# Performance work log

Measured on AMD Instinct MI355X. Metric: run time of the kernel, lower is better.

Reference implementation:

```python
import jax, jax.numpy as jnp
import numpy as np

# Module hyperparameters (match init_kwargs)
D, H1, H2, H3 = 64, 16, 16, 16
N = 65536  # batch size


def _masks():
    # Block-diagonal masks in (in, out) orientation; matches torch m1..m4
    eye = np.eye(D, dtype=np.float32)
    m1 = np.kron(eye, np.ones((1, H1), np.float32))    # (D, H1*D)
    m2 = np.kron(eye, np.ones((H1, H2), np.float32))   # (H1*D, H2*D)
    m3 = np.kron(eye, np.ones((H2, H3), np.float32))   # (H2*D, H3*D)
    m4 = np.kron(eye, np.ones((H3, 1), np.float32))    # (H3*D, D)
    return tuple(jnp.asarray(m) for m in (m1, m2, m3, m4))


def setup_inputs() -> dict:
    key = jax.random.key(0)
    ks = jax.random.split(key, 8)
    def init_w(k, fan_in, fan_out):
        # kaiming-uniform-like scale (nn.Linear default ~ U(-1/sqrt(fan_in), 1/sqrt(fan_in)))
        bound = 1.0 / np.sqrt(fan_in)
        return jax.random.uniform(k, (fan_in, fan_out), jnp.float32, -bound, bound)
    x = jax.random.normal(ks[0], (N, D), jnp.float32)
    W1 = init_w(ks[1], D, H1 * D)
    W2 = init_w(ks[2], H1 * D, H2 * D)
    W3 = init_w(ks[3], H2 * D, H3 * D)
    W4 = init_w(ks[4], H3 * D, D)
    Wp = init_w(ks[5], D, 1)
    bp = jax.random.uniform(ks[6], (1,), jnp.float32, -1.0 / np.sqrt(D), 1.0 / np.sqrt(D))
    return {"x": x, "W1": W1, "W2": W2, "W3": W3, "W4": W4, "Wp": Wp, "bp": bp}


def reference(x, W1, W2, W3, W4, Wp, bp):
    M1, M2, M3, M4 = _masks()
    # SparseLayer: masked dense linear (bias=False), then ELU
    o1 = jax.nn.elu(x @ (W1 * M1))    # (N, H1*D)
    o2 = jax.nn.elu(o1 @ (W2 * M2))   # (N, H2*D)
    o3 = jax.nn.elu(o2 @ (W3 * M3))   # (N, H3*D)
    out = o3 @ (W4 * M4)              # (N, D) per-feature GAM contributions
    pred1 = out @ Wp + bp             # (N, 1) final prediction (Identity act)
    return pred1, out
```

## Files before the change

kernel.cpp:

```cpp
#include <hip/hip_runtime.h>


#define BLK 256
#define FG 8
#define SPT 2
#define DTOT 64

__device__ __forceinline__ float getc(float4 v, int i) {
    switch (i & 3) {
        case 0: return v.x;
        case 1: return v.y;
        case 2: return v.z;
        default: return v.w;
    }
}
#define GET16(h0, h1, h2, h3, i) \
    getc((i) < 4 ? (h0) : (i) < 8 ? (h1) : (i) < 12 ? (h2) : (h3), (i))

__device__ __forceinline__ float4 mul4(float s, float4 w) {
    float4 r;
    r.x = s * w.x; r.y = s * w.y; r.z = s * w.z; r.w = s * w.w;
    return r;
}
__device__ __forceinline__ float4 fma4(float s, float4 w, float4 a) {
    a.x = fmaf(s, w.x, a.x); a.y = fmaf(s, w.y, a.y);
    a.z = fmaf(s, w.z, a.z); a.w = fmaf(s, w.w, a.w);
    return a;
}
__device__ __forceinline__ float elu_f(float v) {
    return v > 0.0f ? v : (__expf(v) - 1.0f);
}
__device__ __forceinline__ float4 elu4(float4 v) {
    float4 r;
    r.x = elu_f(v.x); r.y = elu_f(v.y); r.z = elu_f(v.z); r.w = elu_f(v.w);
    return r;
}
__device__ __forceinline__ float dot4(float4 a, float4 b) {
    return fmaf(a.x, b.x, fmaf(a.y, b.y, fmaf(a.z, b.z, a.w * b.w)));
}
__device__ __forceinline__ float4 zero4() {
    float4 r; r.x = 0.f; r.y = 0.f; r.z = 0.f; r.w = 0.f; return r;
}

__device__ __forceinline__ void stage_weights(
    int tid, int d0,
    const float* __restrict__ W1, const float* __restrict__ W2,
    const float* __restrict__ W3, const float* __restrict__ W4,
    float (*w1s)[16], float (*w2s)[16][16], float (*w3s)[16][16], float (*w4s)[16])
{
    if (tid < 128) {
        int dd = tid >> 4, j = tid & 15;
        int d = d0 + dd;
        w1s[dd][j] = W1[d * 1024 + d * 16 + j];
    } else {
        int t = tid - 128;
        int dd = t >> 4, i = t & 15;
        int d = d0 + dd;
        w4s[dd][i] = W4[(d * 16 + i) * 64 + d];
    }
    for (int idx = tid; idx < FG * 256; idx += BLK) {
        int dd = idx >> 8, r = idx & 255;
        int i = r >> 4, j = r & 15;
        int d = d0 + dd;
        size_t base = (size_t)(d * 16 + i) * 1024 + d * 16 + j;
        w2s[dd][i][j] = W2[base];
        w3s[dd][i][j] = W3[base];
    }
}

#define LAYER16(ws)                                                        \
    {                                                                      \
        float4 a0 = zero4(), a1 = zero4(), a2 = zero4(), a3 = zero4();     \
        float4 b0 = zero4(), b1 = zero4(), b2 = zero4(), b3 = zero4();     \
        _Pragma("unroll")                                                  \
        for (int i = 0; i < 16; ++i) {                                     \
            const float hai = GET16(ha0, ha1, ha2, ha3, i);                \
            const float hbi = GET16(hb0, hb1, hb2, hb3, i);                \
            const float4* wp = (const float4*)((ws) + i * 16);             \
            const float4 q0 = wp[0], q1 = wp[1], q2 = wp[2], q3 = wp[3];   \
            a0 = fma4(hai, q0, a0); a1 = fma4(hai, q1, a1);                \
            a2 = fma4(hai, q2, a2); a3 = fma4(hai, q3, a3);                \
            b0 = fma4(hbi, q0, b0); b1 = fma4(hbi, q1, b1);                \
            b2 = fma4(hbi, q2, b2); b3 = fma4(hbi, q3, b3);                \
        }                                                                  \
        ha0 = elu4(a0); ha1 = elu4(a1); ha2 = elu4(a2); ha3 = elu4(a3);    \
        hb0 = elu4(b0); hb1 = elu4(b1); hb2 = elu4(b2); hb3 = elu4(b3);    \
    }


__global__ __launch_bounds__(256) void transpose_in(
    const float* __restrict__ x, float* __restrict__ xt, int nsamp)
{
    __shared__ float t[64][65];
    const int s0 = blockIdx.x * 64;
    const int c = threadIdx.x & 63;
    const int r0 = threadIdx.x >> 6;
    for (int i = r0; i < 64; i += 4)
        t[i][c] = x[(size_t)(s0 + i) * DTOT + c];
    __syncthreads();
    for (int d = r0; d < 64; d += 4)
        xt[(size_t)d * nsamp + s0 + c] = t[c][d];
}

__global__ __launch_bounds__(BLK, 4) void gam_main_t(
    const float* __restrict__ xt, const float* __restrict__ W1,
    const float* __restrict__ W2, const float* __restrict__ W3,
    const float* __restrict__ W4, float* __restrict__ ot, int nsamp)
{
    __shared__ float w1s[FG][16];
    __shared__ float w2s[FG][16][16];
    __shared__ float w3s[FG][16][16];
    __shared__ float w4s[FG][16];

    const int tid = threadIdx.x;
    const int g = blockIdx.x & 7;
    const int chunk = blockIdx.x >> 3;
    const int d0 = g * FG;

    stage_weights(tid, d0, W1, W2, W3, W4, w1s, w2s, w3s, w4s);
    __syncthreads();

    const int s0 = chunk * (BLK * SPT) + tid;
    const int s1 = s0 + BLK;
    if (s0 >= nsamp) return;

    for (int dd = 0; dd < FG; ++dd) {
        const int d = d0 + dd;
        const size_t rowb = (size_t)d * nsamp;
        const float xv0 = xt[rowb + s0];
        const float xv1 = xt[rowb + s1];

        const float4* w1p = (const float4*)&w1s[dd][0];
        const float4 u0 = w1p[0], u1 = w1p[1], u2 = w1p[2], u3 = w1p[3];
        float4 ha0 = elu4(mul4(xv0, u0)), ha1 = elu4(mul4(xv0, u1));
        float4 ha2 = elu4(mul4(xv0, u2)), ha3 = elu4(mul4(xv0, u3));
        float4 hb0 = elu4(mul4(xv1, u0)), hb1 = elu4(mul4(xv1, u1));
        float4 hb2 = elu4(mul4(xv1, u2)), hb3 = elu4(mul4(xv1, u3));

        LAYER16(&w2s[dd][0][0]);
        LAYER16(&w3s[dd][0][0]);

        const float4* w4p = (const float4*)&w4s[dd][0];
        const float4 q0 = w4p[0], q1 = w4p[1], q2 = w4p[2], q3 = w4p[3];
        const float oa = (dot4(ha0, q0) + dot4(ha1, q1)) +
                         (dot4(ha2, q2) + dot4(ha3, q3));
        const float ob = (dot4(hb0, q0) + dot4(hb1, q1)) +
                         (dot4(hb2, q2) + dot4(hb3, q3));
        ot[rowb + s0] = oa;
        ot[rowb + s1] = ob;
    }
}

__global__ __launch_bounds__(256) void finish(
    const float* __restrict__ ot, const float* __restrict__ Wp,
    const float* __restrict__ bp, float* __restrict__ out,
    float* __restrict__ pred, int nsamp)
{
    __shared__ float t[64][65];
    __shared__ float wps[64];
    const int s0 = blockIdx.x * 64;
    const int c = threadIdx.x & 63;
    const int r0 = threadIdx.x >> 6;
    if (threadIdx.x < 64) wps[threadIdx.x] = Wp[threadIdx.x];
    for (int d = r0; d < 64; d += 4)
        t[d][c] = ot[(size_t)d * nsamp + s0 + c];
    __syncthreads();
    for (int i = r0; i < 64; i += 4)
        out[(size_t)(s0 + i) * DTOT + c] = t[c][i];
    if (r0 == 0) {
        float p = bp[0];
#pragma unroll
        for (int d = 0; d < 64; ++d)
            p = fmaf(t[d][c], wps[d], p);
        pred[s0 + c] = p;
    }
}


__global__ __launch_bounds__(BLK, 4) void gam_main_direct(
    const float* __restrict__ x, const float* __restrict__ W1,
    const float* __restrict__ W2, const float* __restrict__ W3,
    const float* __restrict__ W4, float* __restrict__ out, int nsamp)
{
    __shared__ float w1s[FG][16];
    __shared__ float w2s[FG][16][16];
    __shared__ float w3s[FG][16][16];
    __shared__ float w4s[FG][16];

    const int tid = threadIdx.x;
    const int g = blockIdx.x & 7;
    const int chunk = blockIdx.x >> 3;
    const int d0 = g * FG;

    stage_weights(tid, d0, W1, W2, W3, W4, w1s, w2s, w3s, w4s);
    __syncthreads();

    const int s0 = chunk * (BLK * SPT) + tid;
    const int s1 = s0 + BLK;
    if (s0 >= nsamp) return;

    for (int dd = 0; dd < FG; ++dd) {
        const int d = d0 + dd;
        const float xv0 = x[(size_t)s0 * DTOT + d];
        const float xv1 = x[(size_t)s1 * DTOT + d];

        const float4* w1p = (const float4*)&w1s[dd][0];
        const float4 u0 = w1p[0], u1 = w1p[1], u2 = w1p[2], u3 = w1p[3];
        float4 ha0 = elu4(mul4(xv0, u0)), ha1 = elu4(mul4(xv0, u1));
        float4 ha2 = elu4(mul4(xv0, u2)), ha3 = elu4(mul4(xv0, u3));
        float4 hb0 = elu4(mul4(xv1, u0)), hb1 = elu4(mul4(xv1, u1));
        float4 hb2 = elu4(mul4(xv1, u2)), hb3 = elu4(mul4(xv1, u3));

        LAYER16(&w2s[dd][0][0]);
        LAYER16(&w3s[dd][0][0]);

        const float4* w4p = (const float4*)&w4s[dd][0];
        const float4 q0 = w4p[0], q1 = w4p[1], q2 = w4p[2], q3 = w4p[3];
        out[(size_t)s0 * DTOT + d] = (dot4(ha0, q0) + dot4(ha1, q1)) +
                                     (dot4(ha2, q2) + dot4(ha3, q3));
        out[(size_t)s1 * DTOT + d] = (dot4(hb0, q0) + dot4(hb1, q1)) +
                                     (dot4(hb2, q2) + dot4(hb3, q3));
    }
}

__global__ __launch_bounds__(BLK) void gam_pred_direct(
    const float* __restrict__ out, const float* __restrict__ Wp,
    const float* __restrict__ bp, float* __restrict__ pred, int nsamp)
{
    int gid = blockIdx.x * BLK + threadIdx.x;
    int wave = gid >> 6, lane = gid & 63;
    int sub = lane >> 4, li = lane & 15;
    int s = wave * 4 + sub;
    if (s >= nsamp) return;
    float4 wv = ((const float4*)Wp)[li];
    float4 v = ((const float4*)(out + (size_t)s * DTOT))[li];
    float p = v.x * wv.x + v.y * wv.y + v.z * wv.z + v.w * wv.w;
    p += __shfl_xor(p, 1);
    p += __shfl_xor(p, 2);
    p += __shfl_xor(p, 4);
    p += __shfl_xor(p, 8);
    if (li == 0) pred[s] = p + bp[0];
}

extern "C" void kernel_launch(void* const* d_in, const int* in_sizes, int n_in,
                              void* d_out, int out_size, void* d_ws, size_t ws_size,
                              hipStream_t stream) {
    const float* x  = (const float*)d_in[0];
    const float* W1 = (const float*)d_in[1];
    const float* W2 = (const float*)d_in[2];
    const float* W3 = (const float*)d_in[3];
    const float* W4 = (const float*)d_in[4];
    const float* Wp = (const float*)d_in[5];
    const float* bp = (const float*)d_in[6];

    const int nsamp = in_sizes[0] / DTOT;
    float* pred = (float*)d_out;
    float* outm = pred + nsamp;

    const size_t need = (size_t)2 * nsamp * DTOT * sizeof(float);
    if (ws_size >= need) {
        float* xt = (float*)d_ws;
        float* ot = xt + (size_t)nsamp * DTOT;
        transpose_in<<<dim3(nsamp / 64), dim3(256), 0, stream>>>(x, xt, nsamp);
        gam_main_t<<<dim3((nsamp / (BLK * SPT)) * 8), dim3(BLK), 0, stream>>>(
            xt, W1, W2, W3, W4, ot, nsamp);
        finish<<<dim3(nsamp / 64), dim3(256), 0, stream>>>(
            ot, Wp, bp, outm, pred, nsamp);
    } else {
        int chunks = nsamp / (BLK * SPT);
        gam_main_direct<<<dim3(chunks * 8), dim3(BLK), 0, stream>>>(
            x, W1, W2, W3, W4, outm, nsamp);
        int nthreads = (nsamp / 4) * 64;
        gam_pred_direct<<<dim3((nthreads + BLK - 1) / BLK), dim3(BLK), 0, stream>>>(
            outm, Wp, bp, pred, nsamp);
    }
}
```

Measured before the change: 94.92 us.

## Read block-diagonal weights directly from global memory instead of LDS staging

The transposed-path main kernel no longer stages the per-feature weight blocks into shared memory behind a barrier. Instead each thread loads W1/W2/W3/W4 through uniform global loads (scalar/cached) inside the loop. It also halves features per block (4 instead of 8), which doubles the grid, drops the occupancy hint from launch bounds and disables unrolling of the feature loop. This removes the staging cost and the syncthreads, but adds repeated global/cache reads of weights on the hot inner loop, including strided W4 loads.

```diff
diff --git a/kernel.cpp b/kernel.cpp
--- a/kernel.cpp
+++ b/kernel.cpp
@@ -2,8 +2,8 @@
 
 
 #define BLK 256
+#define FGF 4
 #define FG 8
-#define SPT 2
 #define DTOT 64
 
 __device__ __forceinline__ float getc(float4 v, int i) {
@@ -42,49 +42,23 @@
     float4 r; r.x = 0.f; r.y = 0.f; r.z = 0.f; r.w = 0.f; return r;
 }
 
-__device__ __forceinline__ void stage_weights(
-    int tid, int d0,
-    const float* __restrict__ W1, const float* __restrict__ W2,
-    const float* __restrict__ W3, const float* __restrict__ W4,
-    float (*w1s)[16], float (*w2s)[16][16], float (*w3s)[16][16], float (*w4s)[16])
-{
-    if (tid < 128) {
-        int dd = tid >> 4, j = tid & 15;
-        int d = d0 + dd;
-        w1s[dd][j] = W1[d * 1024 + d * 16 + j];
-    } else {
-        int t = tid - 128;
-        int dd = t >> 4, i = t & 15;
-        int d = d0 + dd;
-        w4s[dd][i] = W4[(d * 16 + i) * 64 + d];
-    }
-    for (int idx = tid; idx < FG * 256; idx += BLK) {
-        int dd = idx >> 8, r = idx & 255;
-        int i = r >> 4, j = r & 15;
-        int d = d0 + dd;
-        size_t base = (size_t)(d * 16 + i) * 1024 + d * 16 + j;
-        w2s[dd][i][j] = W2[base];
-        w3s[dd][i][j] = W3[base];
-    }
-}
-
-#define LAYER16(ws)                                                        \
-    {                                                                      \
-        float4 a0 = zero4(), a1 = zero4(), a2 = zero4(), a3 = zero4();     \
-        float4 b0 = zero4(), b1 = zero4(), b2 = zero4(), b3 = zero4();     \
-        _Pragma("unroll")                                                  \
-        for (int i = 0; i < 16; ++i) {                                     \
-            const float hai = GET16(ha0, ha1, ha2, ha3, i);                \
-            const float hbi = GET16(hb0, hb1, hb2, hb3, i);                \
-            const float4* wp = (const float4*)((ws) + i * 16);             \
-            const float4 q0 = wp[0], q1 = wp[1], q2 = wp[2], q3 = wp[3];   \
-            a0 = fma4(hai, q0, a0); a1 = fma4(hai, q1, a1);                \
-            a2 = fma4(hai, q2, a2); a3 = fma4(hai, q3, a3);                \
-            b0 = fma4(hbi, q0, b0); b1 = fma4(hbi, q1, b1);                \
-            b2 = fma4(hbi, q2, b2); b3 = fma4(hbi, q3, b3);                \
-        }                                                                  \
-        ha0 = elu4(a0); ha1 = elu4(a1); ha2 = elu4(a2); ha3 = elu4(a3);    \
-        hb0 = elu4(b0); hb1 = elu4(b1); hb2 = elu4(b2); hb3 = elu4(b3);    \
+#define LAYER16G(wbase)                                                     \
+    {                                                                       \
+        float4 a0 = zero4(), a1 = zero4(), a2 = zero4(), a3 = zero4();      \
+        float4 b0 = zero4(), b1 = zero4(), b2 = zero4(), b3 = zero4();      \
+        _Pragma("unroll")                                                   \
+        for (int i = 0; i < 16; ++i) {                                      \
+            const float hai = GET16(ha0, ha1, ha2, ha3, i);                 \
+            const float hbi = GET16(hb0, hb1, hb2, hb3, i);                 \
+            const float4* wp = (const float4*)((wbase) + (size_t)i * 1024); \
+            const float4 q0 = wp[0], q1 = wp[1], q2 = wp[2], q3 = wp[3];    \
+            a0 = fma4(hai, q0, a0); a1 = fma4(hai, q1, a1);                 \
+            a2 = fma4(hai, q2, a2); a3 = fma4(hai, q3, a3);                 \
+            b0 = fma4(hbi, q0, b0); b1 = fma4(hbi, q1, b1);                 \
+            b2 = fma4(hbi, q2, b2); b3 = fma4(hbi, q3, b3);                 \
+        }                                                                   \
+        ha0 = elu4(a0); ha1 = elu4(a1); ha2 = elu4(a2); ha3 = elu4(a3);     \
+        hb0 = elu4(b0); hb1 = elu4(b1); hb2 = elu4(b2); hb3 = elu4(b3);     \
     }
 
 
@@ -102,52 +76,53 @@
         xt[(size_t)d * nsamp + s0 + c] = t[c][d];
 }
 
-__global__ __launch_bounds__(BLK, 4) void gam_main_t(
+__global__ __launch_bounds__(BLK) void gam_main_s(
     const float* __restrict__ xt, const float* __restrict__ W1,
     const float* __restrict__ W2, const float* __restrict__ W3,
     const float* __restrict__ W4, float* __restrict__ ot, int nsamp)
 {
-    __shared__ float w1s[FG][16];
-    __shared__ float w2s[FG][16][16];
-    __shared__ float w3s[FG][16][16];
-    __shared__ float w4s[FG][16];
-
     const int tid = threadIdx.x;
-    const int g = blockIdx.x & 7;
-    const int chunk = blockIdx.x >> 3;
-    const int d0 = g * FG;
-
-    stage_weights(tid, d0, W1, W2, W3, W4, w1s, w2s, w3s, w4s);
-    __syncthreads();
-
-    const int s0 = chunk * (BLK * SPT) + tid;
+    const int g = blockIdx.x & 15;
+    const int chunk = blockIdx.x >> 4;
+    const int d0 = g * FGF;
+
+    const int s0 = chunk * (BLK * 2) + tid;
     const int s1 = s0 + BLK;
     if (s0 >= nsamp) return;
 
-    for (int dd = 0; dd < FG; ++dd) {
+#pragma unroll 1
+    for (int dd = 0; dd < FGF; ++dd) {
         const int d = d0 + dd;
         const size_t rowb = (size_t)d * nsamp;
         const float xv0 = xt[rowb + s0];
         const float xv1 = xt[rowb + s1];
 
-        const float4* w1p = (const float4*)&w1s[dd][0];
-        const float4 u0 = w1p[0], u1 = w1p[1], u2 = w1p[2], u3 = w1p[3];
+        const float* w1p = W1 + (size_t)d * 1024 + d * 16;
+        const float* w2p = W2 + (size_t)d * 16 * 1024 + d * 16;
+        const float* w3p = W3 + (size_t)d * 16 * 1024 + d * 16;
+
+        const float4* u = (const float4*)w1p;
+        const float4 u0 = u[0], u1 = u[1], u2 = u[2], u3 = u[3];
         float4 ha0 = elu4(mul4(xv0, u0)), ha1 = elu4(mul4(xv0, u1));
         float4 ha2 = elu4(mul4(xv0, u2)), ha3 = elu4(mul4(xv0, u3));
         float4 hb0 = elu4(mul4(xv1, u0)), hb1 = elu4(mul4(xv1, u1));
         float4 hb2 = elu4(mul4(xv1, u2)), hb3 = elu4(mul4(xv1, u3));
 
-        LAYER16(&w2s[dd][0][0]);
-        LAYER16(&w3s[dd][0][0]);
-
-        const float4* w4p = (const float4*)&w4s[dd][0];
-        const float4 q0 = w4p[0], q1 = w4p[1], q2 = w4p[2], q3 = w4p[3];
-        const float oa = (dot4(ha0, q0) + dot4(ha1, q1)) +
-                         (dot4(ha2, q2) + dot4(ha3, q3));
-        const float ob = (dot4(hb0, q0) + dot4(hb1, q1)) +
-                         (dot4(hb2, q2) + dot4(hb3, q3));
-        ot[rowb + s0] = oa;
-        ot[rowb + s1] = ob;
+        LAYER16G(w2p);
+        LAYER16G(w3p);
+
+        float oa0 = 0.f, oa1 = 0.f, ob0 = 0.f, ob1 = 0.f;
+#pragma unroll
+        for (int i = 0; i < 16; i += 2) {
+            const float wa = W4[(size_t)(d * 16 + i) * 64 + d];
+            const float wb = W4[(size_t)(d * 16 + i + 1) * 64 + d];
+            oa0 = fmaf(GET16(ha0, ha1, ha2, ha3, i), wa, oa0);
+            ob0 = fmaf(GET16(hb0, hb1, hb2, hb3, i), wa, ob0);
+            oa1 = fmaf(GET16(ha0, ha1, ha2, ha3, i + 1), wb, oa1);
+            ob1 = fmaf(GET16(hb0, hb1, hb2, hb3, i + 1), wb, ob1);
+        }
+        ot[rowb + s0] = oa0 + oa1;
+        ot[rowb + s1] = ob0 + ob1;
     }
 }
 
@@ -177,6 +152,51 @@
 }
 
 
+__device__ __forceinline__ void stage_weights(
+    int tid, int d0,
+    const float* __restrict__ W1, const float* __restrict__ W2,
+    const float* __restrict__ W3, const float* __restrict__ W4,
+    float (*w1s)[16], float (*w2s)[16][16], float (*w3s)[16][16], float (*w4s)[16])
+{
+    if (tid < 128) {
+        int dd = tid >> 4, j = tid & 15;
+        int d = d0 + dd;
+        w1s[dd][j] = W1[d * 1024 + d * 16 + j];
+    } else {
+        int t = tid - 128;
+        int dd = t >> 4, i = t & 15;
+        int d = d0 + dd;
+        w4s[dd][i] = W4[(d * 16 + i) * 64 + d];
+    }
+    for (int idx = tid; idx < FG * 256; idx += BLK) {
+        int dd = idx >> 8, r = idx & 255;
+        int i = r >> 4, j = r & 15;
+        int d = d0 + dd;
+        size_t base = (size_t)(d * 16 + i) * 1024 + d * 16 + j;
+        w2s[dd][i][j] = W2[base];
+        w3s[dd][i][j] = W3[base];
+    }
+}
+
+#define LAYER16L(ws)                                                       \
+    {                                                                      \
+        float4 a0 = zero4(), a1 = zero4(), a2 = zero4(), a3 = zero4();     \
+        float4 b0 = zero4(), b1 = zero4(), b2 = zero4(), b3 = zero4();     \
+        _Pragma("unroll")                                                  \
+        for (int i = 0; i < 16; ++i) {                                     \
+            const float hai = GET16(ha0, ha1, ha2, ha3, i);                \
+            const float hbi = GET16(hb0, hb1, hb2, hb3, i);                \
+            const float4* wp = (const float4*)((ws) + i * 16);             \
+            const float4 q0 = wp[0], q1 = wp[1], q2 = wp[2], q3 = wp[3];   \
+            a0 = fma4(hai, q0, a0); a1 = fma4(hai, q1, a1);                \
+            a2 = fma4(hai, q2, a2); a3 = fma4(hai, q3, a3);                \
+            b0 = fma4(hbi, q0, b0); b1 = fma4(hbi, q1, b1);                \
+            b2 = fma4(hbi, q2, b2); b3 = fma4(hbi, q3, b3);                \
+        }                                                                  \
+        ha0 = elu4(a0); ha1 = elu4(a1); ha2 = elu4(a2); ha3 = elu4(a3);    \
+        hb0 = elu4(b0); hb1 = elu4(b1); hb2 = elu4(b2); hb3 = elu4(b3);    \
+    }
+
 __global__ __launch_bounds__(BLK, 4) void gam_main_direct(
     const float* __restrict__ x, const float* __restrict__ W1,
     const float* __restrict__ W2, const float* __restrict__ W3,
@@ -195,7 +215,7 @@
     stage_weights(tid, d0, W1, W2, W3, W4, w1s, w2s, w3s, w4s);
     __syncthreads();
 
-    const int s0 = chunk * (BLK * SPT) + tid;
+    const int s0 = chunk * (BLK * 2) + tid;
     const int s1 = s0 + BLK;
     if (s0 >= nsamp) return;
 
@@ -211,8 +231,8 @@
         float4 hb0 = elu4(mul4(xv1, u0)), hb1 = elu4(mul4(xv1, u1));
         float4 hb2 = elu4(mul4(xv1, u2)), hb3 = elu4(mul4(xv1, u3));
 
-        LAYER16(&w2s[dd][0][0]);
-        LAYER16(&w3s[dd][0][0]);
+        LAYER16L(&w2s[dd][0][0]);
+        LAYER16L(&w3s[dd][0][0]);
 
         const float4* w4p = (const float4*)&w4s[dd][0];
         const float4 q0 = w4p[0], q1 = w4p[1], q2 = w4p[2], q3 = w4p[3];
@@ -262,12 +282,12 @@
         float* xt = (float*)d_ws;
         float* ot = xt + (size_t)nsamp * DTOT;
         transpose_in<<<dim3(nsamp / 64), dim3(256), 0, stream>>>(x, xt, nsamp);
-        gam_main_t<<<dim3((nsamp / (BLK * SPT)) * 8), dim3(BLK), 0, stream>>>(
+        gam_main_s<<<dim3((nsamp / (BLK * 2)) * 16), dim3(BLK), 0, stream>>>(
             xt, W1, W2, W3, W4, ot, nsamp);
         finish<<<dim3(nsamp / 64), dim3(256), 0, stream>>>(
             ot, Wp, bp, outm, pred, nsamp);
     } else {
-        int chunks = nsamp / (BLK * SPT);
+        int chunks = nsamp / (BLK * 2);
         gam_main_direct<<<dim3(chunks * 8), dim3(BLK), 0, stream>>>(
             x, W1, W2, W3, W4, outm, nsamp);
         int nthreads = (nsamp / 4) * 64;
```

Result: faster. 91.58 us (-3.5%).
